# Kernel tuning notes

Hardware: AMD Instinct MI355X
Metric: run time of the kernel (lower is better)

Reference implementation:

```python
import jax, jax.numpy as jnp
import numpy as np

N, E, F_IN, G, C = 100000, 3200000, 64, 1024, 10
BN_EPS = 1e-5


def _glorot(key, shape):
    fan_in, fan_out = shape[0], shape[1]
    lim = jnp.sqrt(6.0 / (fan_in + fan_out))
    return jax.random.uniform(key, shape, jnp.float32, -lim, lim)


def setup_inputs() -> dict:
    key = jax.random.key(0)
    ks = jax.random.split(key, 20)
    x = jax.random.normal(ks[0], (N, F_IN), jnp.float32)
    edge_index = jax.random.randint(ks[1], (2, E), 0, N, jnp.int64)
    batch = jnp.sort(jax.random.randint(ks[2], (N,), 0, G, jnp.int64))
    p = {
        'W1a': _glorot(ks[3], (F_IN, 128)), 'b1a': jnp.zeros((128,), jnp.float32),
        'W1b': _glorot(ks[4], (128, 128)), 'b1b': jnp.zeros((128,), jnp.float32),
        'g1': jnp.ones((128,), jnp.float32), 'be1': jnp.zeros((128,), jnp.float32),
        'W2a': _glorot(ks[5], (128, 64)), 'b2a': jnp.zeros((64,), jnp.float32),
        'W2b': _glorot(ks[6], (64, 64)), 'b2b': jnp.zeros((64,), jnp.float32),
        'g2': jnp.ones((64,), jnp.float32), 'be2': jnp.zeros((64,), jnp.float32),
        'W3a': _glorot(ks[7], (64, 32)), 'b3a': jnp.zeros((32,), jnp.float32),
        'W3b': _glorot(ks[8], (32, 32)), 'b3b': jnp.zeros((32,), jnp.float32),
        'g3': jnp.ones((32,), jnp.float32), 'be3': jnp.zeros((32,), jnp.float32),
        'Wf1': _glorot(ks[9], (32, 128)), 'bf1': jnp.zeros((128,), jnp.float32),
        'Wf2': _glorot(ks[10], (128, 64)), 'bf2': jnp.zeros((64,), jnp.float32),
        'Wf3': _glorot(ks[11], (64, C)), 'bf3': jnp.zeros((C,), jnp.float32),
    }
    return {'x': x, 'edge_index': edge_index, 'batch': batch, **p}


def _gin(x, src, dst, Wa, ba, Wb, bb):
    # GINConv (eps=0): h = MLP(x + sum_{j->i} x_j)
    agg = jax.ops.segment_sum(x[src], dst, num_segments=N)
    h = jax.nn.relu((x + agg) @ Wa + ba)
    return h @ Wb + bb


def _bn(x, g, b):
    # BatchNorm1d, training-mode batch statistics (biased variance)
    mu = jnp.mean(x, axis=0)
    var = jnp.mean((x - mu) ** 2, axis=0)
    return (x - mu) * jax.lax.rsqrt(var + BN_EPS) * g + b


def reference(x, edge_index, batch,
              W1a, b1a, W1b, b1b, g1, be1,
              W2a, b2a, W2b, b2b, g2, be2,
              W3a, b3a, W3b, b3b, g3, be3,
              Wf1, bf1, Wf2, bf2, Wf3, bf3):
    src, dst = edge_index[0], edge_index[1]
    z = _bn(jax.nn.relu(_gin(x, src, dst, W1a, b1a, W1b, b1b)), g1, be1)
    z = _bn(jax.nn.relu(_gin(z, src, dst, W2a, b2a, W2b, b2b)), g2, be2)
    z = _bn(jax.nn.relu(_gin(z, src, dst, W3a, b3a, W3b, b3b)), g3, be3)
    # global_add_pool over graph ids
    z = jax.ops.segment_sum(z, batch, num_segments=G)  # [G, 32]
    cr = jax.nn.relu(z @ Wf1 + bf1)
    cr = jax.nn.relu(cr @ Wf2 + bf2)  # dropout = identity (eval)
    cr = cr @ Wf3 + bf3
    return cr.reshape(-1, C)
```

## Files before the change

### kernel.cpp

```cpp
#include <hip/hip_runtime.h>

#define BN_EPS 1e-5f

typedef _Float16 f16;
typedef _Float16 f16x8 __attribute__((ext_vector_type(8)));
typedef _Float16 f16x4 __attribute__((ext_vector_type(4)));
typedef float f32x4 __attribute__((ext_vector_type(4)));

#define NBLK 512
#define BSHIFT 8
#define BMASK 255

__device__ __forceinline__ void wfrag_one(const float* __restrict__ W, f16* __restrict__ out,
        int FIN, int FOUT, int f,
        const float* __restrict__ stats, int NC, const float* __restrict__ g, float invN) {
    int j = f & 7;
    int lane = (f >> 3) & 63;
    int tile = f >> 9;
    int NT = FOUT >> 4;
    int t = tile % NT, s = tile / NT;
    int k = s * 32 + (lane >> 4) * 8 + j;
    int n = t * 16 + (lane & 15);
    float w = W[(size_t)k * FOUT + n];
    if (stats) {
        float s1 = 0.0f, s2 = 0.0f;
        for (int c = 0; c < NC; c++) {
            s1 += stats[c * 2 * FIN + k];
            s2 += stats[c * 2 * FIN + FIN + k];
        }
        float mu = s1 * invN;
        float var = fmaxf(s2 * invN - mu * mu, 0.0f);
        w *= rsqrtf(var + BN_EPS) * g[k];
    }
    out[f] = (f16)w;
}

__global__ __launch_bounds__(256) void setup_count(const float4* __restrict__ x,
        f16x4* __restrict__ xh, int n4,
        const float* __restrict__ W1a, f16* __restrict__ Wh1a,
        const float* __restrict__ W1b, f16* __restrict__ Wh1b,
        const float* __restrict__ W2b, f16* __restrict__ Wh2b,
        const float* __restrict__ W3b, f16* __restrict__ Wh3b,
        const int* __restrict__ dst, int* __restrict__ hist,
        int NBK, int CHUNK, int E) {
    __shared__ int lh[512];
    const int BC = (n4 + 255) / 256;
    int bid = blockIdx.x;
    const int t = threadIdx.x;
    if (bid < BC) {
        int i = bid * 256 + t;
        if (i < n4) {
            float4 v = x[i];
            f16x4 o;
            o.x = (f16)v.x; o.y = (f16)v.y; o.z = (f16)v.z; o.w = (f16)v.w;
            xh[i] = o;
        }
        return;
    }
    bid -= BC;
    if (bid < 116) {
        if (bid < 32)       wfrag_one(W1a, Wh1a, 64, 128, bid * 256 + t, nullptr, 1, nullptr, 0.f);
        else if (bid < 96)  wfrag_one(W1b, Wh1b, 128, 128, (bid - 32) * 256 + t, nullptr, 1, nullptr, 0.f);
        else if (bid < 112) wfrag_one(W2b, Wh2b, 64, 64, (bid - 96) * 256 + t, nullptr, 1, nullptr, 0.f);
        else                wfrag_one(W3b, Wh3b, 32, 32, (bid - 112) * 256 + t, nullptr, 1, nullptr, 0.f);
        return;
    }
    const int blk = bid - 116;
    for (int r = t; r < 512; r += 256) lh[r] = 0;
    __syncthreads();
    const int e0 = blk * CHUNK, e1 = min(E, e0 + CHUNK);
    const int nq = (e1 - e0) >> 2;
    const int4* d4 = (const int4*)(dst + e0);
    for (int q = t; q < nq; q += 256) {
        int4 v = d4[q];
        atomicAdd(&lh[v.x >> BSHIFT], 1);
        atomicAdd(&lh[v.y >> BSHIFT], 1);
        atomicAdd(&lh[v.z >> BSHIFT], 1);
        atomicAdd(&lh[v.w >> BSHIFT], 1);
    }
    for (int e = e0 + (nq << 2) + t; e < e1; e += 256) atomicAdd(&lh[dst[e] >> BSHIFT], 1);
    __syncthreads();
    for (int r = t; r < NBK; r += 256) hist[r * NBLK + blk] = lh[r];
}

__global__ __launch_bounds__(512) void bkt_bscan(int* __restrict__ hist,
        int* __restrict__ btot) {
    __shared__ int sh[512];
    const int b = blockIdx.x, t = threadIdx.x;
    int v = hist[b * NBLK + t];
    sh[t] = v;
    __syncthreads();
    for (int d = 1; d < 512; d <<= 1) {
        int u = (t >= d) ? sh[t - d] : 0;
        __syncthreads();
        sh[t] += u;
        __syncthreads();
    }
    hist[b * NBLK + t] = sh[t] - v;
    if (t == 511) btot[b] = sh[511];
}

__global__ __launch_bounds__(512) void bkt_scatter(const int* __restrict__ src,
        const int* __restrict__ dst, const int* __restrict__ hist,
        const int* __restrict__ btot, int* __restrict__ bucketed,
        int NBK, int CHUNK, int E) {
    __shared__ int sc[512];
    __shared__ int lc[512];
    const int blk = blockIdx.x, t = threadIdx.x;
    int v = (t < NBK) ? btot[t] : 0;
    sc[t] = v;
    __syncthreads();
    for (int d = 1; d < 512; d <<= 1) {
        int u = (t >= d) ? sc[t - d] : 0;
        __syncthreads();
        sc[t] += u;
        __syncthreads();
    }
    if (t < NBK) lc[t] = (sc[t] - v) + hist[t * NBLK + blk];
    __syncthreads();
    const int e0 = blk * CHUNK, e1 = min(E, e0 + CHUNK);
    const int nq = (e1 - e0) >> 2;
    const int4* d4 = (const int4*)(dst + e0);
    const int4* s4 = (const int4*)(src + e0);
    for (int q = t; q < nq; q += 512) {
        int4 d = d4[q];
        int4 s = s4[q];
        int sl;
        sl = atomicAdd(&lc[d.x >> BSHIFT], 1); bucketed[sl] = ((d.x & BMASK) << 18) | s.x;
        sl = atomicAdd(&lc[d.y >> BSHIFT], 1); bucketed[sl] = ((d.y & BMASK) << 18) | s.y;
        sl = atomicAdd(&lc[d.z >> BSHIFT], 1); bucketed[sl] = ((d.z & BMASK) << 18) | s.z;
        sl = atomicAdd(&lc[d.w >> BSHIFT], 1); bucketed[sl] = ((d.w & BMASK) << 18) | s.w;
    }
    for (int e = e0 + (nq << 2) + t; e < e1; e += 512) {
        int d = dst[e];
        int slot = atomicAdd(&lc[d >> BSHIFT], 1);
        bucketed[slot] = ((d & BMASK) << 18) | src[e];
    }
}

__global__ __launch_bounds__(512) void bkt_csr(const int* __restrict__ bucketed,
        const int* __restrict__ btot, int* __restrict__ off,
        int* __restrict__ elist, int NBK, int N, int E) {
    __shared__ int sc[512];
    __shared__ int lh[256];
    __shared__ int lc[256];
    __shared__ int sh[256];
    const int b = blockIdx.x, t = threadIdx.x;
    int v = (t < NBK) ? btot[t] : 0;
    sc[t] = v;
    __syncthreads();
    for (int d = 1; d < 512; d <<= 1) {
        int u = (t >= d) ? sc[t - d] : 0;
        __syncthreads();
        sc[t] += u;
        __syncthreads();
    }
    const int cnt  = btot[b];
    const int base = sc[b] - cnt;
    if (b == 0 && t == 0) off[N] = E;
    const int b0 = b << BSHIFT;
    const int R = min(N - b0, 256);
    if (t < 256) lh[t] = 0;
    __syncthreads();
    for (int i = t; i < cnt; i += 512) atomicAdd(&lh[bucketed[base + i] >> 18], 1);
    __syncthreads();
    int v0 = 0;
    if (t < 256) { v0 = lh[t]; sh[t] = v0; }
    __syncthreads();
    for (int d = 1; d < 256; d <<= 1) {
        int u = 0;
        if (t < 256 && t >= d) u = sh[t - d];
        __syncthreads();
        if (t < 256) sh[t] += u;
        __syncthreads();
    }
    if (t < 256) { int ex = sh[t] - v0; lh[t] = ex; lc[t] = ex; }
    __syncthreads();
    if (t < R) off[b0 + t] = base + lh[t];
    for (int i = t; i < cnt; i += 512) {
        int p = bucketed[base + i];
        int rk = atomicAdd(&lc[p >> 18], 1);
        elist[base + rk] = p & 0x3FFFF;
    }
}

template<int F, int FOUT, bool STATS, bool AFFINE, typename OutT>
__global__ __launch_bounds__(256) void gather_gemm(const int* __restrict__ off,
        const int* __restrict__ elist, const f16* __restrict__ in,
        const f16* __restrict__ Wf, const float* __restrict__ bias,
        const float* __restrict__ av, const float* __restrict__ ab,
        OutT* __restrict__ Out, float* __restrict__ stats, int N) {
    constexpr int TPN = F / 8;
    constexpr int NPB = 256 / TPN;
    constexpr int SPB = NPB / 16;
    constexpr int WPS = 4 / SPB;
    constexpr int NTF = FOUT / 16;
    constexpr int NTW = NTF / WPS;
    constexpr int NS = F / 32;
    constexpr int LDW = F + 8;
    __shared__ f16 Hl[NPB * LDW];
    __shared__ float Ss[STATS ? 2 * FOUT : 1];
    if (STATS) for (int z = threadIdx.x; z < 2 * FOUT; z += 256) Ss[z] = 0.0f;

    const int base = blockIdx.x * NPB;
    const int rl = threadIdx.x / TPN;
    const int i = base + rl;
    const int l = threadIdx.x & (TPN - 1);
    if (i < N) {
        const int j0 = l * 8;
        const f16x8* __restrict__ inv = (const f16x8*)in;
        f16x8 s = inv[(size_t)i * TPN + l];
        float a[8];
#pragma unroll
        for (int u = 0; u < 8; u++) a[u] = (float)s[u];
        int k = off[i], e = off[i + 1];
        const float cnt = (float)(e - k + 1);
        f16x8 c0, c1, c2, c3;
        if (k + 4 <= e) {
            c0 = inv[(size_t)elist[k + 0] * TPN + l];
            c1 = inv[(size_t)elist[k + 1] * TPN + l];
            c2 = inv[(size_t)elist[k + 2] * TPN + l];
            c3 = inv[(size_t)elist[k + 3] * TPN + l];
            k += 4;
            for (; k + 4 <= e; k += 4) {
                f16x8 d0 = inv[(size_t)elist[k + 0] * TPN + l];
                f16x8 d1 = inv[(size_t)elist[k + 1] * TPN + l];
                f16x8 d2 = inv[(size_t)elist[k + 2] * TPN + l];
                f16x8 d3 = inv[(size_t)elist[k + 3] * TPN + l];
#pragma unroll
                for (int u = 0; u < 8; u++)
                    a[u] += ((float)c0[u] + (float)c1[u]) + ((float)c2[u] + (float)c3[u]);
                c0 = d0; c1 = d1; c2 = d2; c3 = d3;
            }
#pragma unroll
            for (int u = 0; u < 8; u++)
                a[u] += ((float)c0[u] + (float)c1[u]) + ((float)c2[u] + (float)c3[u]);
        }
        for (; k < e; k++) {
            f16x8 p = inv[(size_t)elist[k] * TPN + l];
#pragma unroll
            for (int u = 0; u < 8; u++) a[u] += (float)p[u];
        }
        if (AFFINE) {
            float4 vv0 = *(const float4*)(av + j0);
            float4 vv1 = *(const float4*)(av + j0 + 4);
            float4 bb0 = *(const float4*)(ab + j0);
            float4 bb1 = *(const float4*)(ab + j0 + 4);
            a[0] = fmaxf(fmaf(cnt, vv0.x, a[0] + bb0.x), 0.0f);
            a[1] = fmaxf(fmaf(cnt, vv0.y, a[1] + bb0.y), 0.0f);
            a[2] = fmaxf(fmaf(cnt, vv0.z, a[2] + bb0.z), 0.0f);
            a[3] = fmaxf(fmaf(cnt, vv0.w, a[3] + bb0.w), 0.0f);
            a[4] = fmaxf(fmaf(cnt, vv1.x, a[4] + bb1.x), 0.0f);
            a[5] = fmaxf(fmaf(cnt, vv1.y, a[5] + bb1.y), 0.0f);
            a[6] = fmaxf(fmaf(cnt, vv1.z, a[6] + bb1.z), 0.0f);
            a[7] = fmaxf(fmaf(cnt, vv1.w, a[7] + bb1.w), 0.0f);
        }
        f16x8 o;
#pragma unroll
        for (int u = 0; u < 8; u++) o[u] = (f16)a[u];
        *(f16x8*)&Hl[rl * LDW + j0] = o;
    }
    __syncthreads();

    const int wid = threadIdx.x >> 6;
    const int lane = threadIdx.x & 63;
    const int col = lane & 15;
    const int quad = lane >> 4;
    const int sid = wid / WPS;
    const int cg = wid % WPS;
    const int m0 = base + sid * 16;
    if (m0 < N) {
        f16x8 Bf[NS][NTW];
#pragma unroll
        for (int s = 0; s < NS; s++)
#pragma unroll
            for (int t = 0; t < NTW; t++)
                Bf[s][t] = *(const f16x8*)&Wf[((s * NTF + cg * NTW + t) << 9) + (lane << 3)];
        f32x4 acc[NTW];
#pragma unroll
        for (int t = 0; t < NTW; t++) {
            float b = bias[(cg * NTW + t) * 16 + col];
            acc[t] = (f32x4){b, b, b, b};
        }
        f16x8 Af[NS];
        const int rbase = (sid * 16 + col) * LDW + quad * 8;
#pragma unroll
        for (int s = 0; s < NS; s++) Af[s] = *(const f16x8*)&Hl[rbase + s * 32];
#pragma unroll
        for (int t = 0; t < NTW; t++)
#pragma unroll
            for (int s = 0; s < NS; s++)
                acc[t] = __builtin_amdgcn_mfma_f32_16x16x32_f16(Af[s], Bf[s][t], acc[t], 0, 0, 0);
#pragma unroll
        for (int t = 0; t < NTW; t++) {
            float v0 = fmaxf(acc[t][0], 0.0f);
            float v1 = fmaxf(acc[t][1], 0.0f);
            float v2 = fmaxf(acc[t][2], 0.0f);
            float v3 = fmaxf(acc[t][3], 0.0f);
            OutT* o = Out + (size_t)(m0 + quad * 4) * FOUT + (cg * NTW + t) * 16 + col;
            o[0]        = (OutT)v0;
            o[FOUT]     = (OutT)v1;
            o[2 * FOUT] = (OutT)v2;
            o[3 * FOUT] = (OutT)v3;
            if (STATS) {
                float s1 = (v0 + v1) + (v2 + v3);
                float s2 = (v0 * v0 + v1 * v1) + (v2 * v2 + v3 * v3);
                s1 += __shfl_xor(s1, 16); s1 += __shfl_xor(s1, 32);
                s2 += __shfl_xor(s2, 16); s2 += __shfl_xor(s2, 32);
                if (quad == 0) {
                    atomicAdd(&Ss[(cg * NTW + t) * 16 + col], s1);
                    atomicAdd(&Ss[FOUT + (cg * NTW + t) * 16 + col], s2);
                }
            }
        }
    }
    if (STATS) {
        __syncthreads();
        float* stc = stats + (blockIdx.x & 7) * 2 * FOUT;
        for (int z = threadIdx.x; z < 2 * FOUT; z += 256) atomicAdd(&stc[z], Ss[z]);
    }
}

__global__ __launch_bounds__(256) void layerprep_kernel(const float* __restrict__ W,
        f16* __restrict__ Wh, int FIN, int FOUT,
        const float* __restrict__ stats, int NC, const float* __restrict__ g,
        const float* __restrict__ be, float* __restrict__ v, float invN) {
    if (blockIdx.x == 0) {
        int j = threadIdx.x;
        if (j >= FOUT) return;
        float acc = 0.0f;
        for (int k = 0; k < FIN; k++) {
            float s1 = 0.0f, s2 = 0.0f;
            for (int c = 0; c < NC; c++) {
                s1 += stats[c * 2 * FIN + k];
                s2 += stats[c * 2 * FIN + FIN + k];
            }
            float mu = s1 * invN;
            float var = fmaxf(s2 * invN - mu * mu, 0.0f);
            float sc = rsqrtf(var + BN_EPS) * g[k];
            float sh = be[k] - mu * sc;
            acc = fmaf(sh, W[(size_t)k * FOUT + j], acc);
        }
        v[j] = acc;
        return;
    }
    int f = (blockIdx.x - 1) * 256 + threadIdx.x;
    if (f < FIN * FOUT) wfrag_one(W, Wh, FIN, FOUT, f, stats, NC, g, invN);
}

template<int FIN, int FOUT, int CT, bool STATS, bool RELU, bool BIAS, typename OutT>
__global__ __launch_bounds__(256) void gemm_mfma(const f16* __restrict__ A,
        const f16* __restrict__ Wf, const float* __restrict__ bias,
        OutT* __restrict__ Out, float* __restrict__ stats, int N) {
    constexpr int NS = FIN / 32;
    constexpr int NTF = FOUT / 16;
    constexpr int NT = CT / 16;
    constexpr int NCB = FOUT / CT;
    __shared__ float Ss[STATS ? 2 * CT : 1];
    if (STATS) {
        for (int i = threadIdx.x; i < 2 * CT; i += 256) Ss[i] = 0.0f;
        __syncthreads();
    }
    const int cb = blockIdx.x % NCB;
    const int rb = blockIdx.x / NCB;
    const int RB = gridDim.x / NCB;
    const int t0 = cb * NT;
    const int wid = threadIdx.x >> 6;
    const int lane = threadIdx.x & 63;
    const int col = lane & 15;
    const int quad = lane >> 4;

    f16x8 Bf[NS][NT];
#pragma unroll
    for (int s = 0; s < NS; s++)
#pragma unroll
        for (int t = 0; t < NT; t++)
            Bf[s][t] = *(const f16x8*)&Wf[((s * NTF + t0 + t) << 9) + (lane << 3)];

    float bj[NT];
#pragma unroll
    for (int t = 0; t < NT; t++) bj[t] = BIAS ? bias[(t0 + t) * 16 + col] : 0.0f;

    float ls[NT], ls2[NT];
#pragma unroll
    for (int t = 0; t < NT; t++) { ls[t] = 0.0f; ls2[t] = 0.0f; }

    const int S = N >> 4;
    for (int sidx = rb * 4 + wid; sidx < S; sidx += RB * 4) {
        const int m0 = sidx << 4;
        const f16* a0 = A + (size_t)(m0 + col) * FIN + (quad << 3);
        f16x8 Af[NS];
#pragma unroll
        for (int s = 0; s < NS; s++) Af[s] = *(const f16x8*)(a0 + s * 32);
        f32x4 acc[NT];
#pragma unroll
        for (int t = 0; t < NT; t++) acc[t] = (f32x4){bj[t], bj[t], bj[t], bj[t]};
#pragma unroll
        for (int t = 0; t < NT; t++)
#pragma unroll
            for (int s = 0; s < NS; s++)
                acc[t] = __builtin_amdgcn_mfma_f32_16x16x32_f16(Af[s], Bf[s][t], acc[t], 0, 0, 0);
#pragma unroll
        for (int t = 0; t < NT; t++) {
            float v0 = acc[t][0], v1 = acc[t][1], v2 = acc[t][2], v3 = acc[t][3];
            if (RELU) {
                v0 = fmaxf(v0, 0.0f); v1 = fmaxf(v1, 0.0f);
                v2 = fmaxf(v2, 0.0f); v3 = fmaxf(v3, 0.0f);
            }
            if (STATS) {
                ls[t]  += (v0 + v1) + (v2 + v3);
                ls2[t] += (v0 * v0 + v1 * v1) + (v2 * v2 + v3 * v3);
            }
            OutT* o = Out + (size_t)(m0 + quad * 4) * FOUT + (t0 + t) * 16 + col;
            o[0]        = (OutT)v0;
            o[FOUT]     = (OutT)v1;
            o[2 * FOUT] = (OutT)v2;
            o[3 * FOUT] = (OutT)v3;
        }
    }

    if (STATS) {
#pragma unroll
        for (int t = 0; t < NT; t++) {
            float s1 = ls[t], s2 = ls2[t];
            s1 += __shfl_xor(s1, 16); s1 += __shfl_xor(s1, 32);
            s2 += __shfl_xor(s2, 16); s2 += __shfl_xor(s2, 32);
            if (quad == 0) {
                atomicAdd(&Ss[t * 16 + col], s1);
                atomicAdd(&Ss[CT + t * 16 + col], s2);
            }
        }
        __syncthreads();
        for (int i = threadIdx.x; i < CT; i += 256) {
            atomicAdd(&stats[cb * CT + i], Ss[i]);
            atomicAdd(&stats[FOUT + cb * CT + i], Ss[CT + i]);
        }
    }
}

__global__ __launch_bounds__(256) void bn_pool_kernel(const float* __restrict__ y,
        const float* __restrict__ stats, int NC, const float* __restrict__ gw,
        const float* __restrict__ bw, const int* __restrict__ batch,
        float* __restrict__ pool, int N, float invN) {
    constexpr int F = 32, CH = 64;
    int q = threadIdx.x >> 5;
    int j = threadIdx.x & 31;
    int r0 = (blockIdx.x * 8 + q) * CH;
    if (r0 >= N) return;
    int r1 = min(r0 + CH, N);
    float s1 = 0.0f, s2 = 0.0f;
    for (int c = 0; c < NC; c++) {
        s1 += stats[c * 2 * F + j];
        s2 += stats[c * 2 * F + F + j];
    }
    float mu = s1 * invN;
    float var = fmaxf(s2 * invN - mu * mu, 0.0f);
    float sc = rsqrtf(var + BN_EPS) * gw[j];
    float sh = bw[j] - mu * sc;
    int curg = batch[r0];
    float acc = 0.0f;
    for (int r = r0; r < r1; r++) {
        int g = batch[r];
        if (g != curg) {
            atomicAdd(pool + (size_t)curg * 32 + j, acc);
            acc = 0.0f;
            curg = g;
        }
        acc = fmaf(y[(size_t)r * 32 + j], sc, sh + acc);
    }
    atomicAdd(pool + (size_t)curg * 32 + j, acc);
}

__global__ __launch_bounds__(128) void fc_kernel(const float* __restrict__ pool,
        const float* __restrict__ Wf1, const float* __restrict__ bf1,
        const float* __restrict__ Wf2, const float* __restrict__ bf2,
        const float* __restrict__ Wf3, const float* __restrict__ bf3,
        float* __restrict__ out) {
    __shared__ float zin[32];
    __shared__ float h1[128];
    __shared__ float h2[64];
    const int gidx = blockIdx.x;
    const int t = threadIdx.x;
    if (t < 32) zin[t] = pool[(size_t)gidx * 32 + t];
    __syncthreads();
    {
        float a = bf1[t];
        for (int k = 0; k < 32; k++) a = fmaf(zin[k], Wf1[k * 128 + t], a);
        h1[t] = fmaxf(a, 0.0f);
    }
    __syncthreads();
    if (t < 64) {
        float a = bf2[t];
        for (int k = 0; k < 128; k++) a = fmaf(h1[k], Wf2[k * 64 + t], a);
        h2[t] = fmaxf(a, 0.0f);
    }
    __syncthreads();
    if (t < 10) {
        float a = bf3[t];
        for (int k = 0; k < 64; k++) a = fmaf(h2[k], Wf3[k * 10 + t], a);
        out[(size_t)gidx * 10 + t] = a;
    }
}

extern "C" void kernel_launch(void* const* d_in, const int* in_sizes, int n_in,
                              void* d_out, int out_size, void* d_ws, size_t ws_size,
                              hipStream_t stream) {
    const float* x   = (const float*)d_in[0];
    const int*  ei   = (const int*)d_in[1];
    const int*  batch= (const int*)d_in[2];
    const float* W1a = (const float*)d_in[3];  const float* b1a = (const float*)d_in[4];
    const float* W1b = (const float*)d_in[5];  const float* b1b = (const float*)d_in[6];
    const float* g1  = (const float*)d_in[7];  const float* be1 = (const float*)d_in[8];
    const float* W2a = (const float*)d_in[9];  const float* b2a = (const float*)d_in[10];
    const float* W2b = (const float*)d_in[11]; const float* b2b = (const float*)d_in[12];
    const float* g2  = (const float*)d_in[13]; const float* be2 = (const float*)d_in[14];
    const float* W3a = (const float*)d_in[15]; const float* b3a = (const float*)d_in[16];
    const float* W3b = (const float*)d_in[17]; const float* b3b = (const float*)d_in[18];
    const float* g3  = (const float*)d_in[19]; const float* be3 = (const float*)d_in[20];
    const float* Wf1 = (const float*)d_in[21]; const float* bf1 = (const float*)d_in[22];
    const float* Wf2 = (const float*)d_in[23]; const float* bf2 = (const float*)d_in[24];
    const float* Wf3 = (const float*)d_in[25]; const float* bf3 = (const float*)d_in[26];

    const int N = in_sizes[2];
    const int E = in_sizes[1] / 2;
    const int G = out_size / 10;
    const int* src = ei;
    const int* dst = ei + E;

    const int NBK = (N + BMASK) >> BSHIFT;
    const int CHUNK = (((E + NBLK - 1) / NBLK) + 3) & ~3;

    float* B0   = (float*)d_ws;
    float* B1   = B0 + (size_t)N * 128;
    float* pool = B1 + (size_t)N * 128;
    float* st1  = pool + (size_t)G * 32;
    float* st2c = st1 + 256;
    float* st3c = st2c + 1024;
    int* off    = (int*)(st3c + 512);
    int* elist  = off + (N + 1);
    float* v2   = (float*)(elist + E);
    float* v3   = v2 + 64;
    int* btot   = (int*)(v3 + 32);
    f16* Wh1a   = (f16*)(btot + NBK);
    f16* Wh1b   = Wh1a + 64 * 128;
    f16* Wh2a   = Wh1b + 128 * 128;
    f16* Wh2b   = Wh2a + 128 * 64;
    f16* Wh3a   = Wh2b + 64 * 64;
    f16* Wh3b   = Wh3a + 64 * 32;

    int* bucketed = (int*)B1;
    int* hist     = bucketed + E;

    f16* xh    = (f16*)B0;
    f16* H1    = (f16*)B0 + (size_t)N * 64;
    f16* Y1    = (f16*)B1 + (size_t)N * 64;
    f16* Z1    = (f16*)B0;
    f16* Y2    = (f16*)B0 + (size_t)N * 64;
    f16* Z2    = (f16*)B0;
    float* Y3  = B1 + (size_t)N * 64;

    hipMemsetAsync(pool, 0, ((size_t)G * 32 + 256 + 1024 + 512) * sizeof(float), stream);

    const float invN = 1.0f / (float)N;
    const int GG = 640;

    {
        int BC = (N * 16 + 255) / 256;
        setup_count<<<BC + 116 + NBLK, 256, 0, stream>>>(
            (const float4*)x, (f16x4*)xh, N * 16,
            W1a, Wh1a, W1b, Wh1b, W2b, Wh2b, W3b, Wh3b,
            dst, hist, NBK, CHUNK, E);
    }

    bkt_bscan  <<<NBK, 512, 0, stream>>>(hist, btot);
    bkt_scatter<<<NBLK, 512, 0, stream>>>(src, dst, hist, btot, bucketed, NBK, CHUNK, E);
    bkt_csr    <<<NBK, 512, 0, stream>>>(bucketed, btot, off, elist, NBK, N, E);

    gather_gemm<64, 128, false, false, f16><<<(N + 31) / 32, 256, 0, stream>>>(
        off, elist, xh, Wh1a, b1a, nullptr, nullptr, H1, nullptr, N);
    gemm_mfma<128, 128, 64, true, true, true, f16><<<GG, 256, 0, stream>>>(H1, Wh1b, b1b, Y1, st1, N);

    layerprep_kernel<<<33, 256, 0, stream>>>(W2a, Wh2a, 128, 64, st1, 1, g1, be1, v2, invN);
    gemm_mfma<128, 64, 64, false, false, false, f16><<<GG, 256, 0, stream>>>(Y1, Wh2a, nullptr, Z1, nullptr, N);
    gather_gemm<64, 64, true, true, f16><<<(N + 31) / 32, 256, 0, stream>>>(
        off, elist, Z1, Wh2b, b2b, v2, b2a, Y2, st2c, N);

    layerprep_kernel<<<9, 256, 0, stream>>>(W3a, Wh3a, 64, 32, st2c, 8, g2, be2, v3, invN);
    gemm_mfma<64, 32, 32, false, false, false, f16><<<GG, 256, 0, stream>>>(Y2, Wh3a, nullptr, Z2, nullptr, N);
    gather_gemm<32, 32, true, true, float><<<(N + 63) / 64, 256, 0, stream>>>(
        off, elist, Z2, Wh3b, b3b, v3, b3a, Y3, st3c, N);

    bn_pool_kernel<<<(N + 511) / 512, 256, 0, stream>>>(Y3, st3c, 8, g3, be3, batch, pool, N, invN);

    fc_kernel<<<G, 128, 0, stream>>>(pool, Wf1, bf1, Wf2, bf2, Wf3, bf3, (float*)d_out);
}
```

Measured before the change: 495.3 us.

## Loop all column blocks per GEMM block, stripe BN stats, deepen gather unroll

The gather loop now keeps six neighbour rows in flight instead of four, with a four-row step and a scalar tail for the remainder, to expose more memory-level parallelism. The MFMA GEMM no longer splits output columns across blocks. Each block loads its A fragment once and loops over every column block, reloading the weight fragments inside that loop, which cuts redundant A reads. BN statistics from the first GEMM are spread over 8 striped copies to reduce global atomic contention, and the consumer reads 8 copies. In exchange there are more weight-fragment loads per row tile and higher register pressure.

```diff
diff --git a/kernel.cpp b/kernel.cpp
--- a/kernel.cpp
+++ b/kernel.cpp
@@ -215,23 +215,38 @@
         for (int u = 0; u < 8; u++) a[u] = (float)s[u];
         int k = off[i], e = off[i + 1];
         const float cnt = (float)(e - k + 1);
-        f16x8 c0, c1, c2, c3;
-        if (k + 4 <= e) {
-            c0 = inv[(size_t)elist[k + 0] * TPN + l];
-            c1 = inv[(size_t)elist[k + 1] * TPN + l];
-            c2 = inv[(size_t)elist[k + 2] * TPN + l];
-            c3 = inv[(size_t)elist[k + 3] * TPN + l];
-            k += 4;
-            for (; k + 4 <= e; k += 4) {
+        if (k + 6 <= e) {
+            f16x8 c0 = inv[(size_t)elist[k + 0] * TPN + l];
+            f16x8 c1 = inv[(size_t)elist[k + 1] * TPN + l];
+            f16x8 c2 = inv[(size_t)elist[k + 2] * TPN + l];
+            f16x8 c3 = inv[(size_t)elist[k + 3] * TPN + l];
+            f16x8 c4 = inv[(size_t)elist[k + 4] * TPN + l];
+            f16x8 c5 = inv[(size_t)elist[k + 5] * TPN + l];
+            k += 6;
+            for (; k + 6 <= e; k += 6) {
                 f16x8 d0 = inv[(size_t)elist[k + 0] * TPN + l];
                 f16x8 d1 = inv[(size_t)elist[k + 1] * TPN + l];
                 f16x8 d2 = inv[(size_t)elist[k + 2] * TPN + l];
                 f16x8 d3 = inv[(size_t)elist[k + 3] * TPN + l];
+                f16x8 d4 = inv[(size_t)elist[k + 4] * TPN + l];
+                f16x8 d5 = inv[(size_t)elist[k + 5] * TPN + l];
 #pragma unroll
                 for (int u = 0; u < 8; u++)
-                    a[u] += ((float)c0[u] + (float)c1[u]) + ((float)c2[u] + (float)c3[u]);
-                c0 = d0; c1 = d1; c2 = d2; c3 = d3;
+                    a[u] += (((float)c0[u] + (float)c1[u]) + ((float)c2[u] + (float)c3[u]))
+                          + ((float)c4[u] + (float)c5[u]);
+                c0 = d0; c1 = d1; c2 = d2; c3 = d3; c4 = d4; c5 = d5;
             }
+#pragma unroll
+            for (int u = 0; u < 8; u++)
+                a[u] += (((float)c0[u] + (float)c1[u]) + ((float)c2[u] + (float)c3[u]))
+                      + ((float)c4[u] + (float)c5[u]);
+        }
+        if (k + 4 <= e) {
+            f16x8 c0 = inv[(size_t)elist[k + 0] * TPN + l];
+            f16x8 c1 = inv[(size_t)elist[k + 1] * TPN + l];
+            f16x8 c2 = inv[(size_t)elist[k + 2] * TPN + l];
+            f16x8 c3 = inv[(size_t)elist[k + 3] * TPN + l];
+            k += 4;
 #pragma unroll
             for (int u = 0; u < 8; u++)
                 a[u] += ((float)c0[u] + (float)c1[u]) + ((float)c2[u] + (float)c3[u]);
@@ -356,34 +371,30 @@
     constexpr int NTF = FOUT / 16;
     constexpr int NT = CT / 16;
     constexpr int NCB = FOUT / CT;
-    __shared__ float Ss[STATS ? 2 * CT : 1];
+    __shared__ float Ss[STATS ? 2 * FOUT : 1];
     if (STATS) {
-        for (int i = threadIdx.x; i < 2 * CT; i += 256) Ss[i] = 0.0f;
-        __syncthreads();
-    }
-    const int cb = blockIdx.x % NCB;
-    const int rb = blockIdx.x / NCB;
-    const int RB = gridDim.x / NCB;
-    const int t0 = cb * NT;
+        for (int i = threadIdx.x; i < 2 * FOUT; i += 256) Ss[i] = 0.0f;
+        __syncthreads();
+    }
+    const int rb = blockIdx.x;
+    const int RB = gridDim.x;
     const int wid = threadIdx.x >> 6;
     const int lane = threadIdx.x & 63;
     const int col = lane & 15;
     const int quad = lane >> 4;
 
-    f16x8 Bf[NS][NT];
-#pragma unroll
-    for (int s = 0; s < NS; s++)
+    float bj[NCB][NT];
+#pragma unroll
+    for (int cb = 0; cb < NCB; cb++)
 #pragma unroll
         for (int t = 0; t < NT; t++)
-            Bf[s][t] = *(const f16x8*)&Wf[((s * NTF + t0 + t) << 9) + (lane << 3)];
-
-    float bj[NT];
-#pragma unroll
-    for (int t = 0; t < NT; t++) bj[t] = BIAS ? bias[(t0 + t) * 16 + col] : 0.0f;
-
-    float ls[NT], ls2[NT];
-#pragma unroll
-    for (int t = 0; t < NT; t++) { ls[t] = 0.0f; ls2[t] = 0.0f; }
+            bj[cb][t] = BIAS ? bias[(cb * NT + t) * 16 + col] : 0.0f;
+
+    float ls[NCB][NT], ls2[NCB][NT];
+#pragma unroll
+    for (int cb = 0; cb < NCB; cb++)
+#pragma unroll
+        for (int t = 0; t < NT; t++) { ls[cb][t] = 0.0f; ls2[cb][t] = 0.0f; }
 
     const int S = N >> 4;
     for (int sidx = rb * 4 + wid; sidx < S; sidx += RB * 4) {
@@ -392,49 +403,59 @@
         f16x8 Af[NS];
 #pragma unroll
         for (int s = 0; s < NS; s++) Af[s] = *(const f16x8*)(a0 + s * 32);
-        f32x4 acc[NT];
-#pragma unroll
-        for (int t = 0; t < NT; t++) acc[t] = (f32x4){bj[t], bj[t], bj[t], bj[t]};
-#pragma unroll
-        for (int t = 0; t < NT; t++)
+#pragma unroll
+        for (int cb = 0; cb < NCB; cb++) {
+            const int t0 = cb * NT;
+            f16x8 Bf[NS][NT];
 #pragma unroll
             for (int s = 0; s < NS; s++)
-                acc[t] = __builtin_amdgcn_mfma_f32_16x16x32_f16(Af[s], Bf[s][t], acc[t], 0, 0, 0);
-#pragma unroll
-        for (int t = 0; t < NT; t++) {
-            float v0 = acc[t][0], v1 = acc[t][1], v2 = acc[t][2], v3 = acc[t][3];
-            if (RELU) {
-                v0 = fmaxf(v0, 0.0f); v1 = fmaxf(v1, 0.0f);
-                v2 = fmaxf(v2, 0.0f); v3 = fmaxf(v3, 0.0f);
+#pragma unroll
+                for (int t = 0; t < NT; t++)
+                    Bf[s][t] = *(const f16x8*)&Wf[((s * NTF + t0 + t) << 9) + (lane << 3)];
+            f32x4 acc[NT];
+#pragma unroll
+            for (int t = 0; t < NT; t++) acc[t] = (f32x4){bj[cb][t], bj[cb][t], bj[cb][t], bj[cb][t]};
+#pragma unroll
+            for (int t = 0; t < NT; t++)
+#pragma unroll
+                for (int s = 0; s < NS; s++)
+                    acc[t] = __builtin_amdgcn_mfma_f32_16x16x32_f16(Af[s], Bf[s][t], acc[t], 0, 0, 0);
+#pragma unroll
+            for (int t = 0; t < NT; t++) {
+                float v0 = acc[t][0], v1 = acc[t][1], v2 = acc[t][2], v3 = acc[t][3];
+                if (RELU) {
+                    v0 = fmaxf(v0, 0.0f); v1 = fmaxf(v1, 0.0f);
+                    v2 = fmaxf(v2, 0.0f); v3 = fmaxf(v3, 0.0f);
+                }
+                if (STATS) {
+                    ls[cb][t]  += (v0 + v1) + (v2 + v3);
+                    ls2[cb][t] += (v0 * v0 + v1 * v1) + (v2 * v2 + v3 * v3);
+                }
+                OutT* o = Out + (size_t)(m0 + quad * 4) * FOUT + (t0 + t) * 16 + col;
+                o[0]        = (OutT)v0;
+                o[FOUT]     = (OutT)v1;
+                o[2 * FOUT] = (OutT)v2;
+                o[3 * FOUT] = (OutT)v3;
             }
-            if (STATS) {
-                ls[t]  += (v0 + v1) + (v2 + v3);
-                ls2[t] += (v0 * v0 + v1 * v1) + (v2 * v2 + v3 * v3);
+        }
+    }
+
+    if (STATS) {
+#pragma unroll
+        for (int cb = 0; cb < NCB; cb++)
+#pragma unroll
+            for (int t = 0; t < NT; t++) {
+                float s1 = ls[cb][t], s2 = ls2[cb][t];
+                s1 += __shfl_xor(s1, 16); s1 += __shfl_xor(s1, 32);
+                s2 += __shfl_xor(s2, 16); s2 += __shfl_xor(s2, 32);
+                if (quad == 0) {
+                    atomicAdd(&Ss[(cb * NT + t) * 16 + col], s1);
+                    atomicAdd(&Ss[FOUT + (cb * NT + t) * 16 + col], s2);
+                }
             }
-            OutT* o = Out + (size_t)(m0 + quad * 4) * FOUT + (t0 + t) * 16 + col;
-            o[0]        = (OutT)v0;
-            o[FOUT]     = (OutT)v1;
-            o[2 * FOUT] = (OutT)v2;
-            o[3 * FOUT] = (OutT)v3;
-        }
-    }
-
-    if (STATS) {
-#pragma unroll
-        for (int t = 0; t < NT; t++) {
-            float s1 = ls[t], s2 = ls2[t];
-            s1 += __shfl_xor(s1, 16); s1 += __shfl_xor(s1, 32);
-            s2 += __shfl_xor(s2, 16); s2 += __shfl_xor(s2, 32);
-            if (quad == 0) {
-                atomicAdd(&Ss[t * 16 + col], s1);
-                atomicAdd(&Ss[CT + t * 16 + col], s2);
-            }
-        }
-        __syncthreads();
-        for (int i = threadIdx.x; i < CT; i += 256) {
-            atomicAdd(&stats[cb * CT + i], Ss[i]);
-            atomicAdd(&stats[FOUT + cb * CT + i], Ss[CT + i]);
-        }
+        __syncthreads();
+        float* stc = stats + (blockIdx.x & 7) * 2 * FOUT;
+        for (int i = threadIdx.x; i < 2 * FOUT; i += 256) atomicAdd(&stc[i], Ss[i]);
     }
 }
 
@@ -534,7 +555,7 @@
     float* B1   = B0 + (size_t)N * 128;
     float* pool = B1 + (size_t)N * 128;
     float* st1  = pool + (size_t)G * 32;
-    float* st2c = st1 + 256;
+    float* st2c = st1 + 2048;
     float* st3c = st2c + 1024;
     int* off    = (int*)(st3c + 512);
     int* elist  = off + (N + 1);
@@ -559,7 +580,7 @@
     f16* Z2    = (f16*)B0;
     float* Y3  = B1 + (size_t)N * 64;
 
-    hipMemsetAsync(pool, 0, ((size_t)G * 32 + 256 + 1024 + 512) * sizeof(float), stream);
+    hipMemsetAsync(pool, 0, ((size_t)G * 32 + 2048 + 1024 + 512) * sizeof(float), stream);
 
     const float invN = 1.0f / (float)N;
     const int GG = 640;
@@ -580,7 +601,7 @@
         off, elist, xh, Wh1a, b1a, nullptr, nullptr, H1, nullptr, N);
     gemm_mfma<128, 128, 64, true, true, true, f16><<<GG, 256, 0, stream>>>(H1, Wh1b, b1b, Y1, st1, N);
 
-    layerprep_kernel<<<33, 256, 0, stream>>>(W2a, Wh2a, 128, 64, st1, 1, g1, be1, v2, invN);
+    layerprep_kernel<<<33, 256, 0, stream>>>(W2a, Wh2a, 128, 64, st1, 8, g1, be1, v2, invN);
     gemm_mfma<128, 64, 64, false, false, false, f16><<<GG, 256, 0, stream>>>(Y1, Wh2a, nullptr, Z1, nullptr, N);
     gather_gemm<64, 64, true, true, f16><<<(N + 31) / 32, 256, 0, stream>>>(
         off, elist, Z1, Wh2b, b2b, v2, b2a, Y2, st2c, N);
```

Result: slower. 550.3 us (+11.1%).
